# Performance work log

Hardware: AMD Instinct MI355X
Metric: run time of the kernel (lower is better)

Reference implementation:

```python
import jax, jax.numpy as jnp
import numpy as np

B, S, D = 4, 4096, 64
NEG = 1e31  # matches the torch module's -1e+31 masking constant


def setup_inputs() -> dict:
    key = jax.random.key(0)
    kq, kk, kv = jax.random.split(key, 3)
    return {
        "query": jax.random.normal(kq, (B, S, D), dtype=jnp.float32),
        "key": jax.random.normal(kk, (B, S, D), dtype=jnp.float32),
        "value": jax.random.normal(kv, (B, S, D), dtype=jnp.float32),
    }


def reference(query, key, value):
    # scores: [B, Sq, Sk]
    attn_weights = jnp.einsum("bqd,bkd->bqk", query, key)
    # NOTE: original subtracts the causal penalty BEFORE the sqrt(d) scaling
    Sq, Sk = query.shape[1], key.shape[1]
    causal_mask = jnp.triu(jnp.ones((Sq, Sk), dtype=attn_weights.dtype), k=1)
    attn_weights = attn_weights - causal_mask[None, :, :] * NEG
    attn_weights = attn_weights / np.sqrt(key.shape[-1]).astype(np.float32)
    attn_weights = jax.nn.softmax(attn_weights, axis=-1)
    # dropout p=0.0 -> identity on value
    attn_vec = jnp.einsum("bqk,bkd->bqd", attn_weights, value)
    return attn_vec, attn_weights
```

## Files before the change

kernel.cpp:

```cpp
#include <hip/hip_runtime.h>

#define SQ 4096
#define DD 64
#define NB 4
#define NEL (NB*SQ*DD)

typedef __attribute__((ext_vector_type(4))) float f32x4;
typedef __attribute__((ext_vector_type(8))) __bf16 bf16x8;

__device__ __forceinline__ unsigned short f2bf(float f) {
  unsigned int u = __builtin_bit_cast(unsigned int, f);
  u = (u + 0x7FFFu + ((u >> 16) & 1u)) >> 16;
  return (unsigned short)u;
}

__device__ __forceinline__ bf16x8 ldfrag(const unsigned short* p) {
  uint4 u = *(const uint4*)p;
  return __builtin_bit_cast(bf16x8, u);
}

__device__ __forceinline__ bf16x8 pack_bf8(f32x4 a, f32x4 b) {
  union { unsigned short us[8]; bf16x8 v; } u;
  u.us[0] = f2bf(a[0]); u.us[1] = f2bf(a[1]);
  u.us[2] = f2bf(a[2]); u.us[3] = f2bf(a[3]);
  u.us[4] = f2bf(b[0]); u.us[5] = f2bf(b[1]);
  u.us[6] = f2bf(b[2]); u.us[7] = f2bf(b[3]);
  return u.v;
}

__global__ __launch_bounds__(256) void prep_kernel(
    const float* __restrict__ q, const float* __restrict__ k,
    const float* __restrict__ v, unsigned short* __restrict__ ws)
{
  unsigned short* qbf = ws;
  unsigned short* kbf = ws + (size_t)NEL;
  unsigned short* vt  = ws + 2*(size_t)NEL;
  const int bid = blockIdx.x;
  const int tid = threadIdx.x;
  if (bid < 1024) {
    const float* src = (bid < 512) ? q : k;
    unsigned short* dst = (bid < 512) ? qbf : kbf;
    const int base = (bid & 511) * 512 + tid;
#pragma unroll
    for (int i = 0; i < 2; ++i) {
      int idx = base + i * 256;
      float4 f = ((const float4*)src)[idx];
      ushort4 o;
      o.x = f2bf(f.x); o.y = f2bf(f.y); o.z = f2bf(f.z); o.w = f2bf(f.w);
      ((ushort4*)dst)[idx] = o;
    }
  } else {
    __shared__ unsigned short tile[64][66];
    const int t  = bid - 1024;
    const int bb = t >> 6;
    const int st = t & 63;
    const float* vb = v + (size_t)bb * SQ * DD + (size_t)st * 64 * DD;
    const int r  = tid >> 4;
    const int c4 = tid & 15;
#pragma unroll
    for (int j = 0; j < 4; ++j) {
      int row = r + j * 16;
      float4 f = ((const float4*)(vb + (size_t)row * DD))[c4];
      tile[row][c4 * 4 + 0] = f2bf(f.x);
      tile[row][c4 * 4 + 1] = f2bf(f.y);
      tile[row][c4 * 4 + 2] = f2bf(f.z);
      tile[row][c4 * 4 + 3] = f2bf(f.w);
    }
    __syncthreads();
    unsigned short* vtb = vt + (size_t)bb * DD * SQ;
#pragma unroll
    for (int j = 0; j < 4; ++j) {
      int d   = r + j * 16;
      int s0l = c4 * 4;
      ushort4 o;
      o.x = tile[s0l + 0][d];
      o.y = tile[s0l + 1][d];
      o.z = tile[s0l + 2][d];
      o.w = tile[s0l + 3][d];
      ((ushort4*)(vtb + (size_t)d * SQ + st * 64))[c4] = o;
    }
  }
}

__global__ __launch_bounds__(256, 4) void attn_kernel(
    const unsigned short* __restrict__ qbf,
    const unsigned short* __restrict__ kbf,
    const unsigned short* __restrict__ vtp,
    float* __restrict__ out_vec,
    float* __restrict__ out_w)
{
  __shared__ __align__(16) float pt[4][16][68];
  __shared__ float lred[4][4][4];

  const int tid  = threadIdx.x;
  const int wave = tid >> 6;
  const int lane = tid & 63;
  const int l16  = lane & 15;
  const int quad = lane >> 4;

  const int bidx = blockIdx.x;
  const int b    = bidx & 3;
  const int qt   = 255 - (bidx >> 2);

  const unsigned short* Qb = qbf + (size_t)b * SQ * DD;
  const unsigned short* Kb = kbf + (size_t)b * SQ * DD;
  const unsigned short* Vt = vtp + (size_t)b * DD * SQ;
  float* Wb = out_w  + (size_t)b * SQ * SQ;
  float* Ob = out_vec + (size_t)b * SQ * DD;

  const int q0    = qt * 16;
  const int rowg0 = q0 + quad * 4;

  bf16x8 aQ0, aQ1;
  {
    const unsigned short* qrow = Qb + (size_t)(q0 + l16) * DD + quad * 8;
    aQ0 = ldfrag(qrow);
    aQ1 = ldfrag(qrow + 32);
  }

  const int nkt = (qt >> 2) + 1;
  const float SC = 0.125f * 1.4426950408889634f;
  const f32x4 zf = {0.f, 0.f, 0.f, 0.f};

  float lsum[4] = {0.f, 0.f, 0.f, 0.f};
  for (int kt = wave; kt < nkt; kt += 4) {
    const int k0 = kt * 64;
    f32x4 acc[4] = {zf, zf, zf, zf};
#pragma unroll
    for (int ct = 0; ct < 4; ++ct) {
      const unsigned short* krow = Kb + (size_t)(k0 + ct * 16 + l16) * DD + quad * 8;
      bf16x8 b0 = ldfrag(krow);
      bf16x8 b1 = ldfrag(krow + 32);
      acc[ct] = __builtin_amdgcn_mfma_f32_16x16x32_bf16(aQ0, b0, acc[ct], 0, 0, 0);
      acc[ct] = __builtin_amdgcn_mfma_f32_16x16x32_bf16(aQ1, b1, acc[ct], 0, 0, 0);
    }
#pragma unroll
    for (int ct = 0; ct < 4; ++ct) {
      const int colg = k0 + ct * 16 + l16;
#pragma unroll
      for (int r = 0; r < 4; ++r) {
        float tt = (colg <= rowg0 + r) ? acc[ct][r] * SC : -1e30f;
        lsum[r] += __builtin_amdgcn_exp2f(tt);
      }
    }
  }
#pragma unroll
  for (int r = 0; r < 4; ++r) {
    float vsum = lsum[r];
    vsum += __shfl_xor(vsum, 1);
    vsum += __shfl_xor(vsum, 2);
    vsum += __shfl_xor(vsum, 4);
    vsum += __shfl_xor(vsum, 8);
    lsum[r] = vsum;
  }
  if (l16 == 0) {
#pragma unroll
    for (int r = 0; r < 4; ++r) lred[wave][quad][r] = lsum[r];
  }
  __syncthreads();
  float inv_l[4];
#pragma unroll
  for (int r = 0; r < 4; ++r)
    inv_l[r] = 1.0f / (lred[0][quad][r] + lred[1][quad][r] +
                       lred[2][quad][r] + lred[3][quad][r]);

  f32x4 accO[4] = {zf, zf, zf, zf};
  for (int kt = wave; kt < nkt; kt += 4) {
    const int k0 = kt * 64;
    f32x4 acc[4] = {zf, zf, zf, zf};
#pragma unroll
    for (int ct = 0; ct < 4; ++ct) {
      const unsigned short* krow = Kb + (size_t)(k0 + ct * 16 + l16) * DD + quad * 8;
      bf16x8 b0 = ldfrag(krow);
      bf16x8 b1 = ldfrag(krow + 32);
      acc[ct] = __builtin_amdgcn_mfma_f32_16x16x32_bf16(aQ0, b0, acc[ct], 0, 0, 0);
      acc[ct] = __builtin_amdgcn_mfma_f32_16x16x32_bf16(aQ1, b1, acc[ct], 0, 0, 0);
    }
#pragma unroll
    for (int ct = 0; ct < 4; ++ct) {
      const int colg = k0 + ct * 16 + l16;
#pragma unroll
      for (int r = 0; r < 4; ++r) {
        float tt = (colg <= rowg0 + r) ? acc[ct][r] * SC : -1e30f;
        pt[wave][quad * 4 + r][ct * 16 + l16] = __builtin_amdgcn_exp2f(tt) * inv_l[r];
      }
    }
#pragma unroll
    for (int i = 0; i < 4; ++i) {
      const int rr = 4 * i + quad;
      f32x4 pv = *(const f32x4*)&pt[wave][rr][l16 * 4];
      __builtin_nontemporal_store(pv,
          (f32x4*)(Wb + (size_t)(q0 + rr) * SQ + k0 + l16 * 4));
    }
    {
      const float* prow = &pt[wave][l16][0];
      f32x4 p0 = *(const f32x4*)(prow + quad * 8);
      f32x4 p1 = *(const f32x4*)(prow + quad * 8 + 4);
      f32x4 p2 = *(const f32x4*)(prow + 32 + quad * 8);
      f32x4 p3 = *(const f32x4*)(prow + 32 + quad * 8 + 4);
      bf16x8 aP0 = pack_bf8(p0, p1);
      bf16x8 aP1 = pack_bf8(p2, p3);
#pragma unroll
      for (int ct = 0; ct < 4; ++ct) {
        const unsigned short* vrow = Vt + (size_t)(ct * 16 + l16) * SQ + k0 + quad * 8;
        bf16x8 b0 = ldfrag(vrow);
        bf16x8 b1 = ldfrag(vrow + 32);
        accO[ct] = __builtin_amdgcn_mfma_f32_16x16x32_bf16(aP0, b0, accO[ct], 0, 0, 0);
        accO[ct] = __builtin_amdgcn_mfma_f32_16x16x32_bf16(aP1, b1, accO[ct], 0, 0, 0);
      }
    }
  }

  float* ow_mine = &pt[wave][0][0];
#pragma unroll
  for (int ct = 0; ct < 4; ++ct)
#pragma unroll
    for (int r = 0; r < 4; ++r)
      ow_mine[(quad * 4 + r) * 64 + ct * 16 + l16] = accO[ct][r];
  __syncthreads();
#pragma unroll
  for (int i = 0; i < 4; ++i) {
    int idx = tid + i * 256;
    int row = idx >> 6, col = idx & 63;
    float s = pt[0][0][row * 64 + col] + pt[1][0][row * 64 + col] +
              pt[2][0][row * 64 + col] + pt[3][0][row * 64 + col];
    Ob[(size_t)(q0 + row) * DD + col] = s;
  }

  const int zc0 = nkt * 64;
  const int nz4 = (SQ - zc0) >> 2;
  if (nz4 > 0) {
    const f32x4 z = {0.f, 0.f, 0.f, 0.f};
    for (int r = 0; r < 16; ++r) {
      f32x4* zp = (f32x4*)(Wb + (size_t)(q0 + r) * SQ + zc0);
      for (int i = tid; i < nz4; i += 256)
        __builtin_nontemporal_store(z, zp + i);
    }
  }
}

extern "C" void kernel_launch(void* const* d_in, const int* in_sizes, int n_in,
                              void* d_out, int out_size, void* d_ws, size_t ws_size,
                              hipStream_t stream) {
  const float* q = (const float*)d_in[0];
  const float* k = (const float*)d_in[1];
  const float* v = (const float*)d_in[2];
  float* out_vec = (float*)d_out;
  float* out_w   = out_vec + (size_t)NB * SQ * DD;
  unsigned short* ws = (unsigned short*)d_ws;

  hipLaunchKernelGGL(prep_kernel, dim3(1280), dim3(256), 0, stream, q, k, v, ws);
  hipLaunchKernelGGL(attn_kernel, dim3(1024), dim3(256), 0, stream,
                     ws, ws + (size_t)NEL, ws + 2 * (size_t)NEL, out_vec, out_w);
}
```

Before: 350.1 us.

## Split attention into separate row-sum and output kernels with eight waves per block

Splits the fused attention kernel in two. The first kernel computes each row's softmax normaliser and stores its negative log to a workspace buffer. The second kernel recomputes the scores, folds the normaliser into the exponent with an fma (dropping the per-element multiply), writes the weights and accumulates P·V. Both kernels use 512-thread blocks with 8 waves splitting the key tiles, and the bf16 pack now uses native casts. This costs an extra launch, a global round-trip for the normalisers and a second read of Q/K, in exchange for more parallelism per block and a cheaper inner loop.

```diff
diff --git a/kernel.cpp b/kernel.cpp
--- a/kernel.cpp
+++ b/kernel.cpp
@@ -20,12 +20,10 @@
 }
 
 __device__ __forceinline__ bf16x8 pack_bf8(f32x4 a, f32x4 b) {
-  union { unsigned short us[8]; bf16x8 v; } u;
-  u.us[0] = f2bf(a[0]); u.us[1] = f2bf(a[1]);
-  u.us[2] = f2bf(a[2]); u.us[3] = f2bf(a[3]);
-  u.us[4] = f2bf(b[0]); u.us[5] = f2bf(b[1]);
-  u.us[6] = f2bf(b[2]); u.us[7] = f2bf(b[3]);
-  return u.v;
+  bf16x8 r;
+  r[0] = (__bf16)a[0]; r[1] = (__bf16)a[1]; r[2] = (__bf16)a[2]; r[3] = (__bf16)a[3];
+  r[4] = (__bf16)b[0]; r[5] = (__bf16)b[1]; r[6] = (__bf16)b[2]; r[7] = (__bf16)b[3];
+  return r;
 }
 
 __global__ __launch_bounds__(256) void prep_kernel(
@@ -82,16 +80,12 @@
   }
 }
 
-__global__ __launch_bounds__(256, 4) void attn_kernel(
+__global__ __launch_bounds__(512, 6) void lsum_kernel(
     const unsigned short* __restrict__ qbf,
     const unsigned short* __restrict__ kbf,
-    const unsigned short* __restrict__ vtp,
-    float* __restrict__ out_vec,
-    float* __restrict__ out_w)
+    float* __restrict__ li2_g)
 {
-  __shared__ __align__(16) float pt[4][16][68];
-  __shared__ float lred[4][4][4];
-
+  __shared__ float lred[8][4][4];
   const int tid  = threadIdx.x;
   const int wave = tid >> 6;
   const int lane = tid & 63;
@@ -104,10 +98,6 @@
 
   const unsigned short* Qb = qbf + (size_t)b * SQ * DD;
   const unsigned short* Kb = kbf + (size_t)b * SQ * DD;
-  const unsigned short* Vt = vtp + (size_t)b * DD * SQ;
-  float* Wb = out_w  + (size_t)b * SQ * SQ;
-  float* Ob = out_vec + (size_t)b * SQ * DD;
-
   const int q0    = qt * 16;
   const int rowg0 = q0 + quad * 4;
 
@@ -123,7 +113,7 @@
   const f32x4 zf = {0.f, 0.f, 0.f, 0.f};
 
   float lsum[4] = {0.f, 0.f, 0.f, 0.f};
-  for (int kt = wave; kt < nkt; kt += 4) {
+  for (int kt = wave; kt < nkt; kt += 8) {
     const int k0 = kt * 64;
     f32x4 acc[4] = {zf, zf, zf, zf};
 #pragma unroll
@@ -146,26 +136,73 @@
   }
 #pragma unroll
   for (int r = 0; r < 4; ++r) {
-    float vsum = lsum[r];
-    vsum += __shfl_xor(vsum, 1);
-    vsum += __shfl_xor(vsum, 2);
-    vsum += __shfl_xor(vsum, 4);
-    vsum += __shfl_xor(vsum, 8);
-    lsum[r] = vsum;
+    float v = lsum[r];
+    v += __shfl_xor(v, 1);
+    v += __shfl_xor(v, 2);
+    v += __shfl_xor(v, 4);
+    v += __shfl_xor(v, 8);
+    lsum[r] = v;
   }
   if (l16 == 0) {
 #pragma unroll
     for (int r = 0; r < 4; ++r) lred[wave][quad][r] = lsum[r];
   }
   __syncthreads();
-  float inv_l[4];
+  if (tid < 16) {
+    float s = 0.f;
+#pragma unroll
+    for (int w = 0; w < 8; ++w) s += lred[w][tid >> 2][tid & 3];
+    li2_g[(size_t)b * SQ + q0 + tid] = -__builtin_amdgcn_logf(s);
+  }
+}
+
+__global__ __launch_bounds__(512, 4) void wo_kernel(
+    const unsigned short* __restrict__ qbf,
+    const unsigned short* __restrict__ kbf,
+    const unsigned short* __restrict__ vtp,
+    const float* __restrict__ li2_g,
+    float* __restrict__ out_vec,
+    float* __restrict__ out_w)
+{
+  __shared__ __align__(16) float pt[8][16][68];
+
+  const int tid  = threadIdx.x;
+  const int wave = tid >> 6;
+  const int lane = tid & 63;
+  const int l16  = lane & 15;
+  const int quad = lane >> 4;
+
+  const int bidx = blockIdx.x;
+  const int b    = bidx & 3;
+  const int qt   = 255 - (bidx >> 2);
+
+  const unsigned short* Qb = qbf + (size_t)b * SQ * DD;
+  const unsigned short* Kb = kbf + (size_t)b * SQ * DD;
+  const unsigned short* Vt = vtp + (size_t)b * DD * SQ;
+  float* Wb = out_w  + (size_t)b * SQ * SQ;
+  float* Ob = out_vec + (size_t)b * SQ * DD;
+
+  const int q0    = qt * 16;
+  const int rowg0 = q0 + quad * 4;
+
+  bf16x8 aQ0, aQ1;
+  {
+    const unsigned short* qrow = Qb + (size_t)(q0 + l16) * DD + quad * 8;
+    aQ0 = ldfrag(qrow);
+    aQ1 = ldfrag(qrow + 32);
+  }
+
+  float li2[4];
 #pragma unroll
   for (int r = 0; r < 4; ++r)
-    inv_l[r] = 1.0f / (lred[0][quad][r] + lred[1][quad][r] +
-                       lred[2][quad][r] + lred[3][quad][r]);
-
+    li2[r] = li2_g[(size_t)b * SQ + rowg0 + r];
+
+  const int nkt = (qt >> 2) + 1;
+  const float SC = 0.125f * 1.4426950408889634f;
+  const f32x4 zf = {0.f, 0.f, 0.f, 0.f};
   f32x4 accO[4] = {zf, zf, zf, zf};
-  for (int kt = wave; kt < nkt; kt += 4) {
+
+  for (int kt = wave; kt < nkt; kt += 8) {
     const int k0 = kt * 64;
     f32x4 acc[4] = {zf, zf, zf, zf};
 #pragma unroll
@@ -181,8 +218,9 @@
       const int colg = k0 + ct * 16 + l16;
 #pragma unroll
       for (int r = 0; r < 4; ++r) {
-        float tt = (colg <= rowg0 + r) ? acc[ct][r] * SC : -1e30f;
-        pt[wave][quad * 4 + r][ct * 16 + l16] = __builtin_amdgcn_exp2f(tt) * inv_l[r];
+        float tt = (colg <= rowg0 + r) ? __builtin_fmaf(acc[ct][r], SC, li2[r])
+                                       : -1e30f;
+        pt[wave][quad * 4 + r][ct * 16 + l16] = __builtin_amdgcn_exp2f(tt);
       }
     }
 #pragma unroll
@@ -219,11 +257,12 @@
       ow_mine[(quad * 4 + r) * 64 + ct * 16 + l16] = accO[ct][r];
   __syncthreads();
 #pragma unroll
-  for (int i = 0; i < 4; ++i) {
-    int idx = tid + i * 256;
+  for (int i = 0; i < 2; ++i) {
+    int idx = tid + i * 512;
     int row = idx >> 6, col = idx & 63;
-    float s = pt[0][0][row * 64 + col] + pt[1][0][row * 64 + col] +
-              pt[2][0][row * 64 + col] + pt[3][0][row * 64 + col];
+    float s = 0.f;
+#pragma unroll
+    for (int w = 0; w < 8; ++w) s += pt[w][0][row * 64 + col];
     Ob[(size_t)(q0 + row) * DD + col] = s;
   }
 
@@ -233,7 +272,7 @@
     const f32x4 z = {0.f, 0.f, 0.f, 0.f};
     for (int r = 0; r < 16; ++r) {
       f32x4* zp = (f32x4*)(Wb + (size_t)(q0 + r) * SQ + zc0);
-      for (int i = tid; i < nz4; i += 256)
+      for (int i = tid; i < nz4; i += 512)
         __builtin_nontemporal_store(z, zp + i);
     }
   }
@@ -248,8 +287,12 @@
   float* out_vec = (float*)d_out;
   float* out_w   = out_vec + (size_t)NB * SQ * DD;
   unsigned short* ws = (unsigned short*)d_ws;
+  float* li2_g = (float*)(ws + 3 * (size_t)NEL);
 
   hipLaunchKernelGGL(prep_kernel, dim3(1280), dim3(256), 0, stream, q, k, v, ws);
-  hipLaunchKernelGGL(attn_kernel, dim3(1024), dim3(256), 0, stream,
-                     ws, ws + (size_t)NEL, ws + 2 * (size_t)NEL, out_vec, out_w);
-}
+  hipLaunchKernelGGL(lsum_kernel, dim3(1024), dim3(512), 0, stream,
+                     ws, ws + (size_t)NEL, li2_g);
+  hipLaunchKernelGGL(wo_kernel, dim3(1024), dim3(512), 0, stream,
+                     ws, ws + (size_t)NEL, ws + 2 * (size_t)NEL,
+                     li2_g, out_vec, out_w);
+}
```

New measurement: 354.0 us. About the same (+1.1%).
